# Optimization experiments

Measured on AMD Instinct MI355X. Metric: run time of the kernel, lower is better.

The kernel has to match this reference:

```python
import jax, jax.numpy as jnp
import numpy as np

B, S, D, H, E, K = 4, 1024, 1024, 16, 8, 2
DH = D // H
FF = 4 * D  # expert hidden dim
EPS = 1e-5


def _layernorm(x, g, b):
    mu = jnp.mean(x, axis=-1, keepdims=True)
    var = jnp.mean(jnp.square(x - mu), axis=-1, keepdims=True)
    return (x - mu) / jnp.sqrt(var + EPS) * g + b


def setup_inputs() -> dict:
    key = jax.random.key(0)
    ks = jax.random.split(key, 16)
    s = 0.02
    return {
        "x": jax.random.normal(ks[0], (B, S, D), jnp.float32),
        "mask": jnp.ones((B, S), jnp.int32),
        "ln1_g": jnp.ones((D,), jnp.float32),
        "ln1_b": jnp.zeros((D,), jnp.float32),
        "ln2_g": jnp.ones((D,), jnp.float32),
        "ln2_b": jnp.zeros((D,), jnp.float32),
        "wq": jax.random.normal(ks[1], (D, D), jnp.float32) * s,
        "bq": jnp.zeros((D,), jnp.float32),
        "wk": jax.random.normal(ks[2], (D, D), jnp.float32) * s,
        "bk": jnp.zeros((D,), jnp.float32),
        "wv": jax.random.normal(ks[3], (D, D), jnp.float32) * s,
        "bv": jnp.zeros((D,), jnp.float32),
        "wo": jax.random.normal(ks[4], (D, D), jnp.float32) * s,
        "bo": jnp.zeros((D,), jnp.float32),
        "w_router": jax.random.normal(ks[5], (D, E), jnp.float32) * s,
        "b_router": jnp.zeros((E,), jnp.float32),
        "w1": jax.random.normal(ks[6], (E, D, FF), jnp.float32) * s,
        "b1": jnp.zeros((E, FF), jnp.float32),
        "w2": jax.random.normal(ks[7], (E, FF, D), jnp.float32) * s,
        "b2": jnp.zeros((E, D), jnp.float32),
    }


def _forward(x, mask, ln1_g, ln1_b, ln2_g, ln2_b, wq, bq, wk, bk, wv, bv,
             wo, bo, w_router, b_router, w1, b1, w2, b2):
    scale = DH ** -0.5
    # --- attention sub-block (pre-LN) ---
    xn = _layernorm(x, ln1_g, ln1_b)
    q = (xn @ wq + bq).reshape(B, S, H, DH).transpose(0, 2, 1, 3)  # [B,H,S,DH]
    k = (xn @ wk + bk).reshape(B, S, H, DH).transpose(0, 2, 1, 3)
    v = (xn @ wv + bv).reshape(B, S, H, DH).transpose(0, 2, 1, 3)
    scores = jnp.einsum('bhqd,bhkd->bhqk', q, k) * scale
    scores = jnp.where(mask[:, None, None, :] == 0, -jnp.inf, scores)
    attn = jax.nn.softmax(scores, axis=-1)
    ao = jnp.einsum('bhqk,bhkd->bhqd', attn, v)
    ao = ao.transpose(0, 2, 1, 3).reshape(B, S, D) @ wo + bo
    x = x + ao  # dropout is identity in eval
    # --- MoE sub-block ---
    xn2 = _layernorm(x, ln2_g, ln2_b)
    logits = xn2 @ w_router + b_router          # [B,S,E]
    top_v, top_i = jax.lax.top_k(logits, K)     # [B,S,K]
    probs = jax.nn.softmax(top_v, axis=-1)      # softmax over top-k logits
    # dense combine weight per expert: sum_k prob_k * onehot(idx_k)
    combine = jnp.sum(jax.nn.one_hot(top_i, E, dtype=xn2.dtype) * probs[..., None], axis=-2)  # [B,S,E]
    h = jax.nn.gelu(jnp.einsum('bsd,edh->ebsh', xn2, w1) + b1[:, None, None, :], approximate=False)
    eo = jnp.einsum('ebsh,ehd->ebsd', h, w2) + b2[:, None, None, :]   # [E,B,S,D]
    moe_out = jnp.einsum('bse,ebsd->bsd', combine, eo)
    return x + moe_out


def reference(x, mask, ln1_g, ln1_b, ln2_g, ln2_b, wq, bq, wk, bk, wv, bv,
              wo, bo, w_router, b_router, w1, b1, w2, b2):
    return _forward(x, mask, ln1_g, ln1_b, ln2_g, ln2_b, wq, bq, wk, bk, wv,
                    bv, wo, bo, w_router, b_router, w1, b1, w2, b2)
```

## Files before the change

### kernel.cpp

```cpp
#include <hip/hip_runtime.h>
#include <hip/hip_bf16.h>
#include <cmath>

typedef __hip_bfloat16 bf16;
typedef float f32x4 __attribute__((ext_vector_type(4)));
typedef int   i32x4 __attribute__((ext_vector_type(4)));

#define DEV static __device__ __forceinline__

constexpr int BB   = 4;
constexpr int SS   = 1024;
constexpr int DM   = 1024;
constexpr int HH   = 16;
constexpr int DHD  = 64;
constexpr int NEXP = 8;
constexpr int FFD  = 4096;
constexpr int NTOK = BB*SS;
constexpr int CAP  = NTOK*2 + NEXP*128;

DEV float bf2f(unsigned short u){ union{unsigned int i; float f;} z; z.i=((unsigned int)u)<<16; return z.f; }
DEV unsigned short f2bf(float f){ bf16 h = __float2bfloat16(f); return __builtin_bit_cast(unsigned short, h); }

DEV void stage16(const void* g, void* lds_base_uniform) {
  __builtin_amdgcn_global_load_lds(
      (const __attribute__((address_space(1))) void*)g,
      (__attribute__((address_space(3))) void*)lds_base_uniform,
      16, 0, 0);
}

template<int BM,int BN,int EPI,bool EXPERT,bool GATHER,bool OUT_SLOT,int NPASS=1,int ZMODE=0>
__global__ __launch_bounds__((BM/64)*(BN/64)*64)
void et_gemm(const bf16* __restrict__ A, const bf16* __restrict__ Bt, void* __restrict__ Cout,
             const float* __restrict__ bias, const float* __restrict__ res,
             int Kdim, int lda, int ldb, int ldc,
             long abs_, long bbs_, long cbs_, float scale,
             const int* __restrict__ pad_off, const int* __restrict__ slots,
             long psA, long psB, float* __restrict__ Cf, int bias_zs)
{
  constexpr int WN = BN/64, WM = BM/64, NW = WM*WN;
  constexpr int CA = (BM/16)/NW, CB = (BN/16)/NW;
  const int tid = threadIdx.x, wid = tid>>6, lane = tid&63;

  const int gx = gridDim.x, gy = gridDim.y;
  const long nwg = (long)gx*gy*gridDim.z;
  long lin = blockIdx.x + (long)gx*(blockIdx.y + (long)gy*blockIdx.z);
  {
    const long q = nwg >> 3, r = nwg & 7;
    const long xcd = lin & 7, idx = lin >> 3;
    lin = (xcd < r ? xcd*(q+1) : r*(q+1) + (xcd-r)*q) + idx;
  }
  const int bxi = (int)(lin % gx);
  const long rem = lin / gx;
  const int byi = (int)(rem % gy);
  const int bzi = (int)(rem / gy);

  const int row0 = bxi*BM, col0 = byi*BN;
  const int z = bzi;
  int off0 = 0;
  if constexpr (EXPERT) {
    off0 = pad_off[z];
    const int rows = pad_off[z+1] - off0;
    if (row0 >= rows) return;
  }
  long coff;
  if constexpr (ZMODE==1) {
    const long hb = (long)(z>>4)*SS*DM + (long)(z&15)*64;
    A += hb; Bt += hb; coff = (long)z*SS*SS;
  } else if constexpr (ZMODE==2) {
    A  += (long)z*SS*SS;
    Bt += (long)z*DHD*SS;
    coff = (long)(z>>4)*SS*DM + (long)(z&15)*64;
  } else {
    if constexpr (!EXPERT) A += (size_t)z * abs_;
    Bt += (size_t)z * bbs_;
    coff = (long)z*cbs_;
  }
  const long bofs = (long)z * bias_zs;

  __shared__ __align__(16) bf16 As[2][BM*32];
  __shared__ __align__(16) bf16 Bs[2][BN*32];

  const int sr = lane>>2;
  const int sk = (lane&3)*8;

  long arow[CA];
  #pragma unroll
  for (int i=0;i<CA;i++){
    const int r = (wid + i*NW)*16 + sr;
    if constexpr (GATHER)      arow[i] = slots[off0 + row0 + r];
    else if constexpr (EXPERT) arow[i] = off0 + row0 + r;
    else                       arow[i] = row0 + r;
  }
  int brow[CB];
  #pragma unroll
  for (int i=0;i<CB;i++) brow[i] = col0 + (wid + i*NW)*16 + sr;

  const int wm = wid / WN, wn = wid % WN;
  const int fr = lane & 15, fg = lane >> 4;

  f32x4 acc[4][4];
  #pragma unroll
  for (int m=0;m<4;m++)
    #pragma unroll
    for (int n=0;n<4;n++) acc[m][n] = (f32x4)(0.f);

  static constexpr int AI[3]={0,0,1};
  static constexpr int BI[3]={0,1,0};

  auto STAGE = [&](int buf, int p, int kt) {
    const bf16* Ap = A  + (long)AI[p]*psA;
    const bf16* Bp = Bt + (long)BI[p]*psB;
    #pragma unroll
    for (int i=0;i<CA;i++)
      stage16(Ap + arow[i]*(long)lda + kt + sk, (void*)&As[buf][(wid + i*NW)*512]);
    #pragma unroll
    for (int i=0;i<CB;i++)
      stage16(Bp + (long)brow[i]*ldb + kt + sk, (void*)&Bs[buf][(wid + i*NW)*512]);
  };

  const int nsteps = NPASS * (Kdim >> 5);
  int cur = 0;
  int np = 0, nk = 0;
  STAGE(0, 0, 0);
  nk = 32;
  __syncthreads();

  for (int s = 0; s < nsteps; s++) {
    if (s + 1 < nsteps) {
      if (nk == Kdim) { nk = 0; np++; }
      STAGE(cur^1, np, nk);
      nk += 32;
    }
    i32x4 av[4], bv[4];
    #pragma unroll
    for (int m=0;m<4;m++) av[m] = *(const i32x4*)&As[cur][(wm*64 + m*16 + fr)*32 + fg*8];
    #pragma unroll
    for (int n=0;n<4;n++) bv[n] = *(const i32x4*)&Bs[cur][(wn*64 + n*16 + fr)*32 + fg*8];
    asm volatile("s_nop 1" ::);
    #pragma unroll
    for (int m=0;m<4;m++)
      #pragma unroll
      for (int n=0;n<4;n++)
        asm("v_mfma_f32_16x16x32_bf16 %0, %1, %2, %0"
            : "+v"(acc[m][n]) : "v"(av[m]), "v"(bv[n]));
    __syncthreads();
    cur ^= 1;
  }

  #pragma unroll
  for (int m=0;m<4;m++)
    #pragma unroll
    for (int n=0;n<4;n++)
      asm volatile("s_nop 7\n\ts_nop 7" : "+v"(acc[m][n]) ::);

  const long rbase = (EXPERT && OUT_SLOT) ? (long)(off0 + row0) : (long)row0;
  #pragma unroll
  for (int m=0;m<4;m++) {
    #pragma unroll
    for (int n=0;n<4;n++) {
      #pragma unroll
      for (int j=0;j<4;j++) {
        const long r = rbase + wm*64 + m*16 + fg*4 + j;
        const long c = col0 + wn*64 + n*16 + fr;
        const size_t ci = (size_t)coff + (size_t)r*ldc + c;
        float v = acc[m][n][j];
        if constexpr (EPI==0) {
          ((bf16*)Cout)[ci] = __float2bfloat16(v + bias[bofs + c]);
        } else if constexpr (EPI==1) {
          ((bf16*)Cout)[ci] = __float2bfloat16(v*scale);
        } else if constexpr (EPI==2) {
          ((float*)Cout)[ci] = v + bias[bofs + c] + res[(size_t)r*ldc + c];
        } else if constexpr (EPI==3) {
          const float t = v + bias[bofs + c];
          ((bf16*)Cout)[ci] = __float2bfloat16(0.5f*t*(1.0f+erff(t*0.70710678118654752f)));
        } else {
          const float t = v + bias[bofs + c];
          ((bf16*)Cout)[ci] = __float2bfloat16(t);
          Cf[ci] = t;
        }
      }
    }
  }
}

template<typename T>
__global__ __launch_bounds__(256)
void et_transpose(const T* __restrict__ in, bf16* __restrict__ outp,
                  int ldin, int ldout, long in_bs, long out_bs)
{
  __shared__ float tile[64][65];
  const int z = blockIdx.z;
  in   += (size_t)z * in_bs;
  outp += (size_t)z * out_bs;
  const int r0 = blockIdx.x*64, c0 = blockIdx.y*64;
  const int tid = threadIdx.x;
  #pragma unroll
  for (int i=0;i<4;i++) {
    const int idx = tid*4 + i*1024;
    const int r = idx>>6, c = idx&63;
    if constexpr (sizeof(T)==4) {
      const float4 v = *(const float4*)&in[(size_t)(r0+r)*ldin + c0 + c];
      tile[r][c]=v.x; tile[r][c+1]=v.y; tile[r][c+2]=v.z; tile[r][c+3]=v.w;
    } else {
      const ushort4 v = *(const ushort4*)&in[(size_t)(r0+r)*ldin + c0 + c];
      tile[r][c]=bf2f(v.x); tile[r][c+1]=bf2f(v.y); tile[r][c+2]=bf2f(v.z); tile[r][c+3]=bf2f(v.w);
    }
  }
  __syncthreads();
  #pragma unroll
  for (int i=0;i<4;i++) {
    const int idx = tid*4 + i*1024;
    const int c = idx>>6, r = idx&63;
    ushort4 o;
    o.x=f2bf(tile[r][c]); o.y=f2bf(tile[r+1][c]); o.z=f2bf(tile[r+2][c]); o.w=f2bf(tile[r+3][c]);
    *(ushort4*)&outp[(size_t)(c0+c)*ldout + r0 + r] = o;
  }
}

template<typename TI, typename TO>
__global__ __launch_bounds__(256)
void k_trans_head(const TI* __restrict__ in, TO* __restrict__ outp)
{
  __shared__ float tile[64][65];
  const int z = blockIdx.z;
  in   += (size_t)(z>>4)*SS*DM + (size_t)(z&15)*64;
  outp += (size_t)z*DHD*SS;
  const int r0 = blockIdx.x*64;
  const int tid = threadIdx.x;
  #pragma unroll
  for (int i=0;i<4;i++) {
    const int idx = tid*4 + i*1024;
    const int r = idx>>6, c = idx&63;
    if constexpr (sizeof(TI)==4) {
      const float4 v = *(const float4*)&in[(size_t)(r0+r)*DM + c];
      tile[r][c]=v.x; tile[r][c+1]=v.y; tile[r][c+2]=v.z; tile[r][c+3]=v.w;
    } else {
      const ushort4 v = *(const ushort4*)&in[(size_t)(r0+r)*DM + c];
      tile[r][c]=bf2f(v.x); tile[r][c+1]=bf2f(v.y); tile[r][c+2]=bf2f(v.z); tile[r][c+3]=bf2f(v.w);
    }
  }
  __syncthreads();
  #pragma unroll
  for (int i=0;i<4;i++) {
    const int idx = tid*4 + i*1024;
    const int c = idx>>6, r = idx&63;
    if constexpr (sizeof(TO)==4) {
      float4 o;
      o.x=tile[r][c]; o.y=tile[r+1][c]; o.z=tile[r+2][c]; o.w=tile[r+3][c];
      *(float4*)&outp[(size_t)c*SS + r0 + r] = o;
    } else {
      ushort4 o;
      o.x=f2bf(tile[r][c]); o.y=f2bf(tile[r+1][c]); o.z=f2bf(tile[r+2][c]); o.w=f2bf(tile[r+3][c]);
      *(ushort4*)&outp[(size_t)c*SS + r0 + r] = o;
    }
  }
}

__global__ __launch_bounds__(256)
void et_transpose2(const float* __restrict__ in, bf16* __restrict__ outp,
                   int ldin, int ldout, long pstride)
{
  __shared__ float tile[64][65];
  const int r0 = blockIdx.x*64, c0 = blockIdx.y*64;
  const int tid = threadIdx.x;
  #pragma unroll
  for (int i=0;i<4;i++) {
    const int idx = tid*4 + i*1024;
    const int r = idx>>6, c = idx&63;
    const float4 v = *(const float4*)&in[(size_t)(r0+r)*ldin + c0 + c];
    tile[r][c]=v.x; tile[r][c+1]=v.y; tile[r][c+2]=v.z; tile[r][c+3]=v.w;
  }
  __syncthreads();
  #pragma unroll
  for (int i=0;i<4;i++) {
    const int idx = tid*4 + i*1024;
    const int c = idx>>6, r = idx&63;
    ushort4 o0, o1;
    unsigned short* p0 = (unsigned short*)&o0;
    unsigned short* p1 = (unsigned short*)&o1;
    #pragma unroll
    for (int j=0;j<4;j++) {
      float v = tile[r+j][c];
      const unsigned short h0 = f2bf(v);
      p0[j] = h0;
      v -= bf2f(h0);
      p1[j] = f2bf(v);
    }
    const size_t oi = (size_t)(c0+c)*ldout + r0 + r;
    *(ushort4*)&outp[oi] = o0;
    *(ushort4*)&outp[oi + pstride] = o1;
  }
}

__global__ __launch_bounds__(256)
void et_ln2(const float* __restrict__ xin, const float* __restrict__ g,
            const float* __restrict__ bsh, bf16* __restrict__ outp, long pstride)
{
  const int row = blockIdx.x, tid = threadIdx.x;
  const float4 v = ((const float4*)(xin + (size_t)row*DM))[tid];
  float s = v.x+v.y+v.z+v.w;
  #pragma unroll
  for (int o=32;o;o>>=1) s += __shfl_xor(s,o);
  __shared__ float s4[4], q4[4];
  if ((tid&63)==0) s4[tid>>6]=s;
  __syncthreads();
  const float mu = (s4[0]+s4[1]+s4[2]+s4[3]) * (1.f/DM);
  const float d0=v.x-mu,d1=v.y-mu,d2=v.z-mu,d3=v.w-mu;
  float q = d0*d0+d1*d1+d2*d2+d3*d3;
  #pragma unroll
  for (int o=32;o;o>>=1) q += __shfl_xor(q,o);
  if ((tid&63)==0) q4[tid>>6]=q;
  __syncthreads();
  const float var = (q4[0]+q4[1]+q4[2]+q4[3]) * (1.f/DM);
  const float rstd = rsqrtf(var + 1e-5f);
  const float4 gg = ((const float4*)g)[tid];
  const float4 bb = ((const float4*)bsh)[tid];
  float of[4];
  of[0] = d0*rstd*gg.x + bb.x;
  of[1] = d1*rstd*gg.y + bb.y;
  of[2] = d2*rstd*gg.z + bb.z;
  of[3] = d3*rstd*gg.w + bb.w;
  ushort4 p0, p1;
  unsigned short* pp0 = (unsigned short*)&p0;
  unsigned short* pp1 = (unsigned short*)&p1;
  #pragma unroll
  for (int k=0;k<4;k++) {
    float vv = of[k];
    const unsigned short h0 = f2bf(vv); pp0[k] = h0;
    vv -= bf2f(h0);
    pp1[k] = f2bf(vv);
  }
  const size_t oi = (size_t)row*DM;
  ((ushort4*)(outp + oi))[tid] = p0;
  ((ushort4*)(outp + pstride + oi))[tid] = p1;
}

__global__ __launch_bounds__(256)
void et_ln(const float* __restrict__ xin, const float* __restrict__ g,
           const float* __restrict__ bsh, bf16* __restrict__ outp)
{
  const int row = blockIdx.x, tid = threadIdx.x;
  const float4 v = ((const float4*)(xin + (size_t)row*DM))[tid];
  float s = v.x+v.y+v.z+v.w;
  #pragma unroll
  for (int o=32;o;o>>=1) s += __shfl_xor(s,o);
  __shared__ float s4[4], q4[4];
  if ((tid&63)==0) s4[tid>>6]=s;
  __syncthreads();
  const float mu = (s4[0]+s4[1]+s4[2]+s4[3]) * (1.f/DM);
  const float d0=v.x-mu,d1=v.y-mu,d2=v.z-mu,d3=v.w-mu;
  float q = d0*d0+d1*d1+d2*d2+d3*d3;
  #pragma unroll
  for (int o=32;o;o>>=1) q += __shfl_xor(q,o);
  if ((tid&63)==0) q4[tid>>6]=q;
  __syncthreads();
  const float var = (q4[0]+q4[1]+q4[2]+q4[3]) * (1.f/DM);
  const float rstd = rsqrtf(var + 1e-5f);
  const float4 gg = ((const float4*)g)[tid];
  const float4 bb = ((const float4*)bsh)[tid];
  ushort4 o4;
  o4.x = f2bf(d0*rstd*gg.x + bb.x);
  o4.y = f2bf(d1*rstd*gg.y + bb.y);
  o4.z = f2bf(d2*rstd*gg.z + bb.z);
  o4.w = f2bf(d3*rstd*gg.w + bb.w);
  ((ushort4*)(outp + (size_t)row*DM))[tid] = o4;
}

__global__ __launch_bounds__(256)
void et_softmax(bf16* __restrict__ scp, const int* __restrict__ mask)
{
  const int row = blockIdx.x, tid = threadIdx.x;
  const int b = row >> 14;
  bf16* rp = scp + (size_t)row*SS;
  const int* mrow = mask + (size_t)b*SS;
  const ushort4 u = ((const ushort4*)rp)[tid];
  const int4 mv = ((const int4*)mrow)[tid];
  float f0 = bf2f(u.x), f1 = bf2f(u.y), f2 = bf2f(u.z), f3 = bf2f(u.w);
  if (mv.x==0) f0 = -1e30f;
  if (mv.y==0) f1 = -1e30f;
  if (mv.z==0) f2 = -1e30f;
  if (mv.w==0) f3 = -1e30f;
  float m = fmaxf(fmaxf(f0,f1),fmaxf(f2,f3));
  #pragma unroll
  for (int o=32;o;o>>=1) m = fmaxf(m, __shfl_xor(m,o));
  __shared__ float sm[4], ssum[4];
  if ((tid&63)==0) sm[tid>>6] = m;
  __syncthreads();
  m = fmaxf(fmaxf(sm[0],sm[1]),fmaxf(sm[2],sm[3]));
  const float e0 = __expf(f0-m), e1 = __expf(f1-m), e2 = __expf(f2-m), e3 = __expf(f3-m);
  float s = e0+e1+e2+e3;
  #pragma unroll
  for (int o=32;o;o>>=1) s += __shfl_xor(s,o);
  if ((tid&63)==0) ssum[tid>>6] = s;
  __syncthreads();
  s = ssum[0]+ssum[1]+ssum[2]+ssum[3];
  const float ri = 1.0f/s;
  ushort4 o4;
  o4.x = f2bf(e0*ri); o4.y = f2bf(e1*ri); o4.z = f2bf(e2*ri); o4.w = f2bf(e3*ri);
  ((ushort4*)rp)[tid] = o4;
}

__global__ __launch_bounds__(256)
void et_router2(const float* __restrict__ x1, const float* __restrict__ g,
                const float* __restrict__ bsh, const float* __restrict__ wr,
                const float* __restrict__ br, int* __restrict__ t2e,
                float* __restrict__ t2p, int* __restrict__ flaglist,
                int* __restrict__ cntb)
{
  const int wid = threadIdx.x>>6, lane = threadIdx.x&63;
  const int t = blockIdx.x*4 + wid;
  const float* xr = x1 + (size_t)t*DM;
  float4 xv[4];
  float s = 0.f;
  #pragma unroll
  for (int p=0;p<4;p++){
    xv[p] = *(const float4*)&xr[p*256 + lane*4];
    s += xv[p].x+xv[p].y+xv[p].z+xv[p].w;
  }
  #pragma unroll
  for (int o=32;o;o>>=1) s += __shfl_xor(s,o);
  const float mu = s * (1.f/DM);
  float q = 0.f;
  #pragma unroll
  for (int p=0;p<4;p++){
    const float a=xv[p].x-mu,b=xv[p].y-mu,c=xv[p].z-mu,d=xv[p].w-mu;
    q += a*a+b*b+c*c+d*d;
  }
  #pragma unroll
  for (int o=32;o;o>>=1) q += __shfl_xor(q,o);
  const float rstd = rsqrtf(q*(1.f/DM) + 1e-5f);
  float acc[NEXP];
  #pragma unroll
  for (int e=0;e<NEXP;e++) acc[e]=0.f;
  #pragma unroll
  for (int p=0;p<4;p++){
    const int d0 = p*256 + lane*4;
    const float4 gg = *(const float4*)&g[d0];
    const float4 bb = *(const float4*)&bsh[d0];
    float xn[4];
    xn[0]=(xv[p].x-mu)*rstd*gg.x+bb.x;
    xn[1]=(xv[p].y-mu)*rstd*gg.y+bb.y;
    xn[2]=(xv[p].z-mu)*rstd*gg.z+bb.z;
    xn[3]=(xv[p].w-mu)*rstd*gg.w+bb.w;
    #pragma unroll
    for (int j=0;j<4;j++){
      const float4 w0  = ((const float4*)&wr[(size_t)(d0+j)*NEXP])[0];
      const float4 w1v = ((const float4*)&wr[(size_t)(d0+j)*NEXP])[1];
      acc[0]+=xn[j]*w0.x;  acc[1]+=xn[j]*w0.y;  acc[2]+=xn[j]*w0.z;  acc[3]+=xn[j]*w0.w;
      acc[4]+=xn[j]*w1v.x; acc[5]+=xn[j]*w1v.y; acc[6]+=xn[j]*w1v.z; acc[7]+=xn[j]*w1v.w;
    }
  }
  #pragma unroll
  for (int e=0;e<NEXP;e++)
    #pragma unroll
    for (int o=32;o;o>>=1) acc[e] += __shfl_xor(acc[e],o);
  if (lane==0) {
    float v0=-1e30f, v1=-1e30f, v2=-1e30f; int e0=0, e1=0;
    #pragma unroll
    for (int e=0;e<NEXP;e++) {
      const float v = acc[e] + br[e];
      if (v>v0){v2=v1;v1=v0;e1=e0;v0=v;e0=e;}
      else if (v>v1){v2=v1;v1=v;e1=e;}
      else if (v>v2){v2=v;}
    }
    const float dd = __expf(v1-v0);
    const float p0 = 1.f/(1.f+dd);
    t2e[t*2]=e0; t2e[t*2+1]=e1;
    t2p[t*2]=p0; t2p[t*2+1]=dd*p0;
    if (v1 - v2 < 0.02f) {
      const int b = t >> 10;
      const int ib = atomicAdd(&cntb[b], 1);
      flaglist[b*1024 + ib] = t;
    }
  }
}

__global__ __launch_bounds__(256)
void k_rec4(const float* __restrict__ qf, const float* __restrict__ kfT,
            const float* __restrict__ vf, const int* __restrict__ flaglist,
            const int* __restrict__ cntb, const int* __restrict__ mask,
            float* __restrict__ aoF)
{
  const int h = blockIdx.y, b = blockIdx.z;
  const int tid = threadIdx.x, lane = tid&63, wv_ = tid>>6;
  const int nb = cntb[b];
  __shared__ float qs[4][64];
  __shared__ float scb[4][SS];
  __shared__ float part[4][4][64];
  __shared__ float tsum[4];
  const int* mrow = mask + (size_t)b*SS;
  const float* kbase = kfT + ((size_t)(b*HH + h)*DHD)*SS + tid;
  const float* vbase = vf + (size_t)b*SS*DM + h*64 + lane;

  for (int t0 = blockIdx.x*4; t0 < nb; t0 += gridDim.x*4) {
    const int nt = min(4, nb - t0);
    for (int idx = tid; idx < 4*64; idx += 256) {
      const int j = idx >> 6, d = idx & 63;
      float qv = 0.f;
      if (j < nt) {
        const int t = flaglist[b*1024 + t0 + j];
        qv = qf[(size_t)t*DM + h*64 + d];
      }
      qs[j][d] = qv;
    }
    __syncthreads();
    float a00=0,a01=0,a02=0,a03=0, a10=0,a11=0,a12=0,a13=0;
    float a20=0,a21=0,a22=0,a23=0, a30=0,a31=0,a32=0,a33=0;
    #pragma unroll 4
    for (int u=0; u<64; u++) {
      const float* kr = kbase + (size_t)u*SS;
      const float k0 = kr[0], k1 = kr[256], k2 = kr[512], k3 = kr[768];
      const float q0 = qs[0][u], q1 = qs[1][u], q2 = qs[2][u], q3 = qs[3][u];
      a00 += q0*k0; a01 += q0*k1; a02 += q0*k2; a03 += q0*k3;
      a10 += q1*k0; a11 += q1*k1; a12 += q1*k2; a13 += q1*k3;
      a20 += q2*k0; a21 += q2*k1; a22 += q2*k2; a23 += q2*k3;
      a30 += q3*k0; a31 += q3*k1; a32 += q3*k2; a33 += q3*k3;
    }
    const bool m0 = mrow[tid]!=0, m1 = mrow[tid+256]!=0, m2 = mrow[tid+512]!=0, m3 = mrow[tid+768]!=0;
    scb[0][tid]=m0?a00*0.125f:-1e30f; scb[0][tid+256]=m1?a01*0.125f:-1e30f;
    scb[0][tid+512]=m2?a02*0.125f:-1e30f; scb[0][tid+768]=m3?a03*0.125f:-1e30f;
    scb[1][tid]=m0?a10*0.125f:-1e30f; scb[1][tid+256]=m1?a11*0.125f:-1e30f;
    scb[1][tid+512]=m2?a12*0.125f:-1e30f; scb[1][tid+768]=m3?a13*0.125f:-1e30f;
    scb[2][tid]=m0?a20*0.125f:-1e30f; scb[2][tid+256]=m1?a21*0.125f:-1e30f;
    scb[2][tid+512]=m2?a22*0.125f:-1e30f; scb[2][tid+768]=m3?a23*0.125f:-1e30f;
    scb[3][tid]=m0?a30*0.125f:-1e30f; scb[3][tid+256]=m1?a31*0.125f:-1e30f;
    scb[3][tid+512]=m2?a32*0.125f:-1e30f; scb[3][tid+768]=m3?a33*0.125f:-1e30f;
    __syncthreads();
    {
      const int j = wv_;
      float v[16];
      float lm = -1e30f;
      #pragma unroll
      for (int kk=0;kk<16;kk++) { v[kk] = scb[j][lane + kk*64]; lm = fmaxf(lm, v[kk]); }
      #pragma unroll
      for (int o=32;o;o>>=1) lm = fmaxf(lm, __shfl_xor(lm,o));
      float ls = 0.f;
      #pragma unroll
      for (int kk=0;kk<16;kk++) {
        const float e = expf(v[kk]-lm);
        scb[j][lane + kk*64] = e; ls += e;
      }
      #pragma unroll
      for (int o=32;o;o>>=1) ls += __shfl_xor(ls,o);
      if (lane==0) tsum[j] = ls;
    }
    __syncthreads();
    float p0=0.f, p1=0.f, p2=0.f, p3=0.f;
    for (int s = wv_*4; s < SS; s += 16) {
      const float v0 = vbase[(size_t) s   *DM];
      const float v1 = vbase[(size_t)(s+1)*DM];
      const float v2 = vbase[(size_t)(s+2)*DM];
      const float v3 = vbase[(size_t)(s+3)*DM];
      p0 += scb[0][s]*v0 + scb[0][s+1]*v1 + scb[0][s+2]*v2 + scb[0][s+3]*v3;
      p1 += scb[1][s]*v0 + scb[1][s+1]*v1 + scb[1][s+2]*v2 + scb[1][s+3]*v3;
      p2 += scb[2][s]*v0 + scb[2][s+1]*v1 + scb[2][s+2]*v2 + scb[2][s+3]*v3;
      p3 += scb[3][s]*v0 + scb[3][s+1]*v1 + scb[3][s+2]*v2 + scb[3][s+3]*v3;
    }
    part[wv_][0][lane] = p0;
    part[wv_][1][lane] = p1;
    part[wv_][2][lane] = p2;
    part[wv_][3][lane] = p3;
    __syncthreads();
    for (int idx = tid; idx < nt*64; idx += 256) {
      const int j = idx >> 6, d = idx & 63;
      aoF[(size_t)(b*1024 + t0 + j)*DM + h*64 + d] =
        (part[0][j][d]+part[1][j][d]+part[2][j][d]+part[3][j][d]) / tsum[j];
    }
    __syncthreads();
  }
}

__global__ __launch_bounds__(256)
void k_flag_proj2(const float* __restrict__ aoF, const float* __restrict__ wo,
                  const float* __restrict__ bo, const float* __restrict__ x,
                  const int* __restrict__ flaglist, const int* __restrict__ cntb,
                  float* __restrict__ yF)
{
  const int tile = blockIdx.x;
  const int b = tile >> 7;
  const int i0 = (tile & 127) * 8;
  const int nb = cntb[b];
  if (i0 >= nb) return;
  const int nt = min(8, nb - i0);
  const int c0 = blockIdx.y * 128;
  const int tid = threadIdx.x;
  const int c = c0 + (tid & 127);
  const int dh = tid >> 7;
  __shared__ float ar[8][DM];
  __shared__ float ph[2][8][128];
  for (int k = tid; k < 8*256; k += 256) {
    const int j = k >> 8, q4i = k & 255;
    float4 v = make_float4(0.f,0.f,0.f,0.f);
    if (j < nt) v = ((const float4*)(aoF + (size_t)(b*1024 + i0 + j)*DM))[q4i];
    ((float4*)ar[j])[q4i] = v;
  }
  __syncthreads();
  float acc0=0.f, acc1=0.f, acc2=0.f, acc3=0.f;
  float acc4=0.f, acc5=0.f, acc6=0.f, acc7=0.f;
  const int dbase = dh*512;
  #pragma unroll 4
  for (int d=0; d<512; d++) {
    const float w = wo[(size_t)(dbase+d)*DM + c];
    acc0 += ar[0][dbase+d]*w; acc1 += ar[1][dbase+d]*w;
    acc2 += ar[2][dbase+d]*w; acc3 += ar[3][dbase+d]*w;
    acc4 += ar[4][dbase+d]*w; acc5 += ar[5][dbase+d]*w;
    acc6 += ar[6][dbase+d]*w; acc7 += ar[7][dbase+d]*w;
  }
  const int lc = tid & 127;
  ph[dh][0][lc]=acc0; ph[dh][1][lc]=acc1; ph[dh][2][lc]=acc2; ph[dh][3][lc]=acc3;
  ph[dh][4][lc]=acc4; ph[dh][5][lc]=acc5; ph[dh][6][lc]=acc6; ph[dh][7][lc]=acc7;
  __syncthreads();
  for (int k = tid; k < nt*128; k += 256) {
    const int j = k >> 7, ccl = k & 127;
    const int cc = c0 + ccl;
    const int slot = b*1024 + i0 + j;
    const int t = flaglist[slot];
    yF[(size_t)slot*DM + cc] = ph[0][j][ccl] + ph[1][j][ccl] + bo[cc] + x[(size_t)t*DM + cc];
  }
}

__global__ __launch_bounds__(256)
void k_flag_router(const float* __restrict__ yF, const float* __restrict__ g,
                   const float* __restrict__ bsh, const float* __restrict__ wr,
                   const float* __restrict__ br, const int* __restrict__ flaglist,
                   const int* __restrict__ cntb, int* __restrict__ t2e,
                   float* __restrict__ t2p)
{
  const int tid = threadIdx.x, lane = tid&63, wv_ = tid>>6;
  __shared__ float s4[4], q4[4], pt[4][8];
  for (int idx = blockIdx.x; idx < NTOK; idx += gridDim.x) {
    const int b = idx >> 10, ib = idx & 1023;
    if (ib >= cntb[b]) continue;
    const int t = flaglist[idx];
    const float4 v = ((const float4*)(yF + (size_t)idx*DM))[tid];
    float s = v.x+v.y+v.z+v.w;
    #pragma unroll
    for (int o=32;o;o>>=1) s += __shfl_xor(s,o);
    if (lane==0) s4[wv_]=s;
    __syncthreads();
    const float mu = (s4[0]+s4[1]+s4[2]+s4[3])*(1.f/DM);
    const float d0=v.x-mu, d1=v.y-mu, d2=v.z-mu, d3=v.w-mu;
    float q = d0*d0+d1*d1+d2*d2+d3*d3;
    #pragma unroll
    for (int o=32;o;o>>=1) q += __shfl_xor(q,o);
    if (lane==0) q4[wv_]=q;
    __syncthreads();
    const float var = (q4[0]+q4[1]+q4[2]+q4[3])*(1.f/DM);
    const float rstd = 1.0f/sqrtf(var + 1e-5f);
    const int dbase = tid*4;
    const float4 gg = ((const float4*)g)[tid];
    const float4 bb = ((const float4*)bsh)[tid];
    const float x0 = d0*rstd*gg.x+bb.x, x1_ = d1*rstd*gg.y+bb.y;
    const float x2 = d2*rstd*gg.z+bb.z, x3_ = d3*rstd*gg.w+bb.w;
    float pl[8];
    #pragma unroll
    for (int e=0;e<8;e++)
      pl[e] = x0*wr[(size_t)(dbase+0)*8+e] + x1_*wr[(size_t)(dbase+1)*8+e]
            + x2*wr[(size_t)(dbase+2)*8+e] + x3_*wr[(size_t)(dbase+3)*8+e];
    #pragma unroll
    for (int e=0;e<8;e++)
      #pragma unroll
      for (int o=32;o;o>>=1) pl[e] += __shfl_xor(pl[e],o);
    if (lane==0) {
      #pragma unroll
      for (int e=0;e<8;e++) pt[wv_][e]=pl[e];
    }
    __syncthreads();
    if (tid==0) {
      float v0=-1e30f, v1=-1e30f; int e0=0, e1=0;
      for (int e=0;e<8;e++) {
        const float L = pt[0][e]+pt[1][e]+pt[2][e]+pt[3][e] + br[e];
        if (L>v0){v1=v0;e1=e0;v0=L;e0=e;}
        else if (L>v1){v1=L;e1=e;}
      }
      const float dd=expf(v1-v0), p0=1.f/(1.f+dd);
      t2e[t*2]=e0; t2e[t*2+1]=e1;
      t2p[t*2]=p0; t2p[t*2+1]=dd*p0;
    }
    __syncthreads();
  }
}

__global__ void et_zero(int* cnt){ if (threadIdx.x < 16) cnt[threadIdx.x]=0; }

__global__ void et_bcat(const float* __restrict__ bq, const float* __restrict__ bk,
                        const float* __restrict__ bv, float* __restrict__ bcat)
{
  const int i = blockIdx.x*256 + threadIdx.x;
  if (i < DM) { bcat[i]=bq[i]; bcat[DM+i]=bk[i]; bcat[2*DM+i]=bv[i]; }
}

__global__ void et_count(const int* __restrict__ t2e, int* __restrict__ cnt)
{
  const int t = blockIdx.x*256 + threadIdx.x;
  if (t < NTOK) {
    atomicAdd(&cnt[t2e[t*2]], 1);
    atomicAdd(&cnt[t2e[t*2+1]], 1);
  }
}

__global__ void et_scan(const int* __restrict__ cnt, int* __restrict__ poff,
                        int* __restrict__ fil, int* __restrict__ slots)
{
  const int tid = threadIdx.x;
  if (tid==0) {
    int o=0;
    for (int e=0;e<NEXP;e++){ poff[e]=o; o += ((cnt[e]+127)>>7)<<7; }
    poff[NEXP]=o;
  }
  if (tid<NEXP) fil[tid]=0;
  for (int i=tid;i<CAP;i+=256) slots[i]=0;
}

__global__ void et_fill(const int* __restrict__ t2e, const int* __restrict__ poff,
                        int* __restrict__ fil, int* __restrict__ slots, int* __restrict__ sof)
{
  const int t = blockIdx.x*256 + threadIdx.x;
  if (t >= NTOK) return;
  #pragma unroll
  for (int kk=0;kk<2;kk++) {
    const int e = t2e[t*2+kk];
    const int pos = atomicAdd(&fil[e], 1);
    const int sl = poff[e] + pos;
    slots[sl] = t;
    sof[t*2+kk] = sl;
  }
}

__global__ __launch_bounds__(256)
void et_combine(const float* __restrict__ x1, const bf16* __restrict__ eo,
                const float* __restrict__ t2p, const int* __restrict__ sof,
                float* __restrict__ outp)
{
  const int t = blockIdx.x, tid = threadIdx.x;
  const int s0 = sof[t*2], s1 = sof[t*2+1];
  const float p0 = t2p[t*2], p1 = t2p[t*2+1];
  const float4 xv = ((const float4*)(x1 + (size_t)t*DM))[tid];
  const ushort4 a = ((const ushort4*)(eo + (size_t)s0*DM))[tid];
  const ushort4 c = ((const ushort4*)(eo + (size_t)s1*DM))[tid];
  float4 o;
  o.x = xv.x + p0*bf2f(a.x) + p1*bf2f(c.x);
  o.y = xv.y + p0*bf2f(a.y) + p1*bf2f(c.y);
  o.z = xv.z + p0*bf2f(a.z) + p1*bf2f(c.z);
  o.w = xv.w + p0*bf2f(a.w) + p1*bf2f(c.w);
  ((float4*)(outp + (size_t)t*DM))[tid] = o;
}

extern "C" void kernel_launch(void* const* d_in, const int* in_sizes, int n_in,
                              void* d_out, int out_size, void* d_ws, size_t ws_size,
                              hipStream_t stream)
{
  (void)in_sizes; (void)n_in; (void)out_size; (void)ws_size;
  const float* x    = (const float*)d_in[0];
  const int*   mask = (const int*)  d_in[1];
  const float* ln1g = (const float*)d_in[2];
  const float* ln1b = (const float*)d_in[3];
  const float* ln2g = (const float*)d_in[4];
  const float* ln2b = (const float*)d_in[5];
  const float* wq   = (const float*)d_in[6];
  const float* bq   = (const float*)d_in[7];
  const float* wk   = (const float*)d_in[8];
  const float* bk   = (const float*)d_in[9];
  const float* wv   = (const float*)d_in[10];
  const float* bv   = (const float*)d_in[11];
  const float* wo   = (const float*)d_in[12];
  const float* bo   = (const float*)d_in[13];
  const float* wr   = (const float*)d_in[14];
  const float* br   = (const float*)d_in[15];
  const float* w1   = (const float*)d_in[16];
  const float* b1   = (const float*)d_in[17];
  const float* w2   = (const float*)d_in[18];
  const float* b2   = (const float*)d_in[19];
  float* outp = (float*)d_out;

  char* wsb = (char*)d_ws;
  size_t off = 0;
  auto alloc = [&](size_t bytes)->void* {
    void* p = wsb + off;
    off += (bytes + 255) & ~(size_t)255;
    return p;
  };
  const long WPS  = (long)DM*DM;
  const long XPS  = (long)NTOK*DM;
  const long EWS  = (long)DM*FFD;
  bf16*  wqT2  = (bf16*) alloc((size_t)2*WPS*2);
  bf16*  wkT2  = (bf16*) alloc((size_t)2*WPS*2);
  bf16*  wvT2  = (bf16*) alloc((size_t)2*WPS*2);
  bf16*  woT   = (bf16*) alloc((size_t)WPS*2);
  bf16*  w1Ta  = (bf16*) alloc((size_t)NEXP*EWS*2);
  bf16*  w2Ta  = (bf16*) alloc((size_t)NEXP*EWS*2);
  bf16*  xn2p  = (bf16*) alloc((size_t)2*XPS*2);
  bf16*  qb    = (bf16*) alloc((size_t)XPS*2);
  bf16*  kb    = (bf16*) alloc((size_t)XPS*2);
  bf16*  vb    = (bf16*) alloc((size_t)XPS*2);
  bf16*  vt    = (bf16*) alloc((size_t)XPS*2);
  float* qf    = (float*)alloc((size_t)XPS*4);
  float* kf    = (float*)alloc((size_t)XPS*4);
  float* vf    = (float*)alloc((size_t)XPS*4);
  float* kfT   = (float*)alloc((size_t)XPS*4);
  bf16*  aob   = (bf16*) alloc((size_t)XPS*2);
  float* x1    = (float*)alloc((size_t)XPS*4);
  bf16*  xn2   = (bf16*) alloc((size_t)XPS*2);
  bf16*  hbuf  = (bf16*) alloc((size_t)CAP*FFD*2);
  bf16*  eo    = (bf16*) alloc((size_t)CAP*DM*2);
  float* bcat  = (float*)alloc((size_t)3*DM*4);
  int*   t2e   = (int*)  alloc((size_t)NTOK*2*4);
  float* t2p   = (float*)alloc((size_t)NTOK*2*4);
  int*   slots = (int*)  alloc((size_t)CAP*4);
  int*   sof   = (int*)  alloc((size_t)NTOK*2*4);
  int*   flagl = (int*)  alloc((size_t)NTOK*4);
  int*   cnt   = (int*)  alloc(64);
  int*   fil   = (int*)  alloc(64);
  int*   poff  = (int*)  alloc(64);
  int*   cntb  = cnt + 8;
  bf16*  sc    = (bf16*) w1Ta;
  float* aoF   = (float*)qb;
  float* yF    = (float*)vb;

  const dim3 T256(256);

  et_zero<<<1,64,0,stream>>>(cnt);
  et_bcat<<<4,T256,0,stream>>>(bq, bk, bv, bcat);
  et_transpose2<<<dim3(DM/64,DM/64),T256,0,stream>>>(wq, wqT2, DM, DM, WPS);
  et_transpose2<<<dim3(DM/64,DM/64),T256,0,stream>>>(wk, wkT2, DM, DM, WPS);
  et_transpose2<<<dim3(DM/64,DM/64),T256,0,stream>>>(wv, wvT2, DM, DM, WPS);
  et_transpose<float><<<dim3(DM/64,DM/64,1),T256,0,stream>>>(wo, woT, DM, DM, 0, 0);

  et_ln2<<<NTOK,T256,0,stream>>>(x, ln1g, ln1b, xn2p, XPS);

  et_gemm<128,64,4,false,false,false,3,0><<<dim3(NTOK/128, DM/64, 3),dim3(128),0,stream>>>(
      xn2p, wqT2, qb, bcat, nullptr, DM, DM, DM, DM,
      0, 2*WPS, XPS, 1.f, nullptr, nullptr, XPS, WPS, qf, DM);

  k_trans_head<bf16,bf16><<<dim3(SS/64,1,BB*HH),T256,0,stream>>>(vb, vt);
  k_trans_head<float,float><<<dim3(SS/64,1,BB*HH),T256,0,stream>>>(kf, kfT);

  et_gemm<128,128,1,false,false,false,1,1><<<dim3(SS/128, SS/128, BB*HH),T256,0,stream>>>(
      qb, kb, sc, nullptr, nullptr, DHD, DM, DM, SS,
      0,0,0, 0.125f, nullptr,nullptr, 0,0,nullptr, 0);
  et_softmax<<<BB*HH*SS,T256,0,stream>>>(sc, mask);
  et_gemm<128,64,1,false,false,false,1,2><<<dim3(SS/128, 1, BB*HH),dim3(128),0,stream>>>(
      sc, vt, aob, nullptr, nullptr, SS, SS, SS, DM,
      0,0,0, 1.0f, nullptr,nullptr, 0,0,nullptr, 0);

  et_gemm<128,128,2,false,false,false,1,0><<<dim3(NTOK/128, DM/128, 1),T256,0,stream>>>(
      aob, woT, x1, bo, x, DM, DM, DM, DM, 0,0,0, 1.f, nullptr,nullptr, 0,0,nullptr, 0);
  et_ln<<<NTOK,T256,0,stream>>>(x1, ln2g, ln2b, xn2);

  et_router2<<<NTOK/4,T256,0,stream>>>(x1, ln2g, ln2b, wr, br, t2e, t2p, flagl, cntb);
  k_rec4<<<dim3(32,HH,BB),T256,0,stream>>>(qf, kfT, vf, flagl, cntb, mask, aoF);
  k_flag_proj2<<<dim3(NTOK/8, DM/128),T256,0,stream>>>(aoF, wo, bo, x, flagl, cntb, yF);
  k_flag_router<<<1024,T256,0,stream>>>(yF, ln2g, ln2b, wr, br, flagl, cntb, t2e, t2p);

  et_count<<<NTOK/256,T256,0,stream>>>(t2e, cnt);
  et_scan<<<1,T256,0,stream>>>(cnt, poff, fil, slots);
  et_fill<<<NTOK/256,T256,0,stream>>>(t2e, poff, fil, slots, sof);

  et_transpose<float><<<dim3(DM/64, FFD/64, NEXP),T256,0,stream>>>(w1, w1Ta, FFD, DM, EWS, EWS);
  et_transpose<float><<<dim3(FFD/64, DM/64, NEXP),T256,0,stream>>>(w2, w2Ta, DM, FFD, EWS, EWS);

  et_gemm<128,128,3,true,true,true,1,0><<<dim3(NTOK/128, FFD/128, NEXP),T256,0,stream>>>(
      xn2, w1Ta, hbuf, b1, nullptr, DM, DM, DM, FFD,
      0, EWS, 0, 1.f, poff, slots, 0,0,nullptr, FFD);
  et_gemm<128,128,0,true,false,true,1,0><<<dim3(NTOK/128, DM/128, NEXP),T256,0,stream>>>(
      hbuf, w2Ta, eo, b2, nullptr, FFD, FFD, FFD, DM,
      0, EWS, 0, 1.f, poff, nullptr, 0,0,nullptr, DM);

  et_combine<<<NTOK,T256,0,stream>>>(x1, eo, t2p, sof, outp);
}
```

Measured before the change: 954.3 us.

## Triple-buffer GEMM LDS staging and fuse second layernorm into router

The shared GEMM kernel moves from double to triple-buffered LDS staging. It uses explicit vmcnt waits and raw s_barrier, so two K-tiles are in flight while the current one is computed, which should hide more global load latency. Separately, the standalone second layernorm kernel is removed and the router kernel now writes the bf16 normalized activations itself, saving a launch and a read of x1. The extra LDS buffer raises shared memory per block and may reduce occupancy.

```diff
diff --git a/kernel.cpp b/kernel.cpp
--- a/kernel.cpp
+++ b/kernel.cpp
@@ -28,6 +28,15 @@
       16, 0, 0);
 }
 
+template<int N> DEV void wait_vmcnt() {
+  if constexpr (N==0)      asm volatile("s_waitcnt vmcnt(0)" ::: "memory");
+  else if constexpr (N==4) asm volatile("s_waitcnt vmcnt(4)" ::: "memory");
+  else if constexpr (N==6) asm volatile("s_waitcnt vmcnt(6)" ::: "memory");
+  else if constexpr (N==8) asm volatile("s_waitcnt vmcnt(8)" ::: "memory");
+  else                     asm volatile("s_waitcnt vmcnt(12)" ::: "memory");
+}
+DEV void block_bar(){ asm volatile("s_barrier" ::: "memory"); }
+
 template<int BM,int BN,int EPI,bool EXPERT,bool GATHER,bool OUT_SLOT,int NPASS=1,int ZMODE=0>
 __global__ __launch_bounds__((BM/64)*(BN/64)*64)
 void et_gemm(const bf16* __restrict__ A, const bf16* __restrict__ Bt, void* __restrict__ Cout,
@@ -39,6 +48,7 @@
 {
   constexpr int WN = BN/64, WM = BM/64, NW = WM*WN;
   constexpr int CA = (BM/16)/NW, CB = (BN/16)/NW;
+  constexpr int LPT = CA + CB;
   const int tid = threadIdx.x, wid = tid>>6, lane = tid&63;
 
   const int gx = gridDim.x, gy = gridDim.y;
@@ -77,8 +87,8 @@
   }
   const long bofs = (long)z * bias_zs;
 
-  __shared__ __align__(16) bf16 As[2][BM*32];
-  __shared__ __align__(16) bf16 Bs[2][BN*32];
+  __shared__ __align__(16) bf16 As[3][BM*32];
+  __shared__ __align__(16) bf16 Bs[3][BN*32];
 
   const int sr = lane>>2;
   const int sk = (lane&3)*8;
@@ -107,29 +117,31 @@
   static constexpr int AI[3]={0,0,1};
   static constexpr int BI[3]={0,1,0};
 
-  auto STAGE = [&](int buf, int p, int kt) {
-    const bf16* Ap = A  + (long)AI[p]*psA;
-    const bf16* Bp = Bt + (long)BI[p]*psB;
+  int np = 0, nk = 0;
+  auto STAGE = [&](int buf) {
+    const bf16* Ap = A  + (long)AI[np]*psA;
+    const bf16* Bp = Bt + (long)BI[np]*psB;
     #pragma unroll
     for (int i=0;i<CA;i++)
-      stage16(Ap + arow[i]*(long)lda + kt + sk, (void*)&As[buf][(wid + i*NW)*512]);
+      stage16(Ap + arow[i]*(long)lda + nk + sk, (void*)&As[buf][(wid + i*NW)*512]);
     #pragma unroll
     for (int i=0;i<CB;i++)
-      stage16(Bp + (long)brow[i]*ldb + kt + sk, (void*)&Bs[buf][(wid + i*NW)*512]);
+      stage16(Bp + (long)brow[i]*ldb + nk + sk, (void*)&Bs[buf][(wid + i*NW)*512]);
+    nk += 32;
+    if (nk == Kdim) { nk = 0; np++; }
   };
 
   const int nsteps = NPASS * (Kdim >> 5);
-  int cur = 0;
-  int np = 0, nk = 0;
-  STAGE(0, 0, 0);
-  nk = 32;
-  __syncthreads();
-
+  STAGE(0);
+  if (nsteps > 1) { STAGE(1); wait_vmcnt<LPT>(); }
+  else            { wait_vmcnt<0>(); }
+  block_bar();
+
+  int cur = 0, sb = 2;
   for (int s = 0; s < nsteps; s++) {
-    if (s + 1 < nsteps) {
-      if (nk == Kdim) { nk = 0; np++; }
-      STAGE(cur^1, np, nk);
-      nk += 32;
+    if (s + 2 < nsteps) {
+      STAGE(sb);
+      sb = (sb==2) ? 0 : sb+1;
     }
     i32x4 av[4], bv[4];
     #pragma unroll
@@ -143,8 +155,10 @@
       for (int n=0;n<4;n++)
         asm("v_mfma_f32_16x16x32_bf16 %0, %1, %2, %0"
             : "+v"(acc[m][n]) : "v"(av[m]), "v"(bv[n]));
-    __syncthreads();
-    cur ^= 1;
+    if (s + 2 < nsteps)      wait_vmcnt<LPT>();
+    else if (s + 1 < nsteps) wait_vmcnt<0>();
+    if (s + 1 < nsteps) block_bar();
+    cur = (cur==2) ? 0 : cur+1;
   }
 
   #pragma unroll
@@ -336,37 +350,6 @@
 }
 
 __global__ __launch_bounds__(256)
-void et_ln(const float* __restrict__ xin, const float* __restrict__ g,
-           const float* __restrict__ bsh, bf16* __restrict__ outp)
-{
-  const int row = blockIdx.x, tid = threadIdx.x;
-  const float4 v = ((const float4*)(xin + (size_t)row*DM))[tid];
-  float s = v.x+v.y+v.z+v.w;
-  #pragma unroll
-  for (int o=32;o;o>>=1) s += __shfl_xor(s,o);
-  __shared__ float s4[4], q4[4];
-  if ((tid&63)==0) s4[tid>>6]=s;
-  __syncthreads();
-  const float mu = (s4[0]+s4[1]+s4[2]+s4[3]) * (1.f/DM);
-  const float d0=v.x-mu,d1=v.y-mu,d2=v.z-mu,d3=v.w-mu;
-  float q = d0*d0+d1*d1+d2*d2+d3*d3;
-  #pragma unroll
-  for (int o=32;o;o>>=1) q += __shfl_xor(q,o);
-  if ((tid&63)==0) q4[tid>>6]=q;
-  __syncthreads();
-  const float var = (q4[0]+q4[1]+q4[2]+q4[3]) * (1.f/DM);
-  const float rstd = rsqrtf(var + 1e-5f);
-  const float4 gg = ((const float4*)g)[tid];
-  const float4 bb = ((const float4*)bsh)[tid];
-  ushort4 o4;
-  o4.x = f2bf(d0*rstd*gg.x + bb.x);
-  o4.y = f2bf(d1*rstd*gg.y + bb.y);
-  o4.z = f2bf(d2*rstd*gg.z + bb.z);
-  o4.w = f2bf(d3*rstd*gg.w + bb.w);
-  ((ushort4*)(outp + (size_t)row*DM))[tid] = o4;
-}
-
-__global__ __launch_bounds__(256)
 void et_softmax(bf16* __restrict__ scp, const int* __restrict__ mask)
 {
   const int row = blockIdx.x, tid = threadIdx.x;
@@ -403,9 +386,9 @@
 __global__ __launch_bounds__(256)
 void et_router2(const float* __restrict__ x1, const float* __restrict__ g,
                 const float* __restrict__ bsh, const float* __restrict__ wr,
-                const float* __restrict__ br, int* __restrict__ t2e,
-                float* __restrict__ t2p, int* __restrict__ flaglist,
-                int* __restrict__ cntb)
+                const float* __restrict__ br, bf16* __restrict__ xn2,
+                int* __restrict__ t2e, float* __restrict__ t2p,
+                int* __restrict__ flaglist, int* __restrict__ cntb)
 {
   const int wid = threadIdx.x>>6, lane = threadIdx.x&63;
   const int t = blockIdx.x*4 + wid;
@@ -442,6 +425,9 @@
     xn[1]=(xv[p].y-mu)*rstd*gg.y+bb.y;
     xn[2]=(xv[p].z-mu)*rstd*gg.z+bb.z;
     xn[3]=(xv[p].w-mu)*rstd*gg.w+bb.w;
+    ushort4 xo;
+    xo.x=f2bf(xn[0]); xo.y=f2bf(xn[1]); xo.z=f2bf(xn[2]); xo.w=f2bf(xn[3]);
+    *(ushort4*)&xn2[(size_t)t*DM + d0] = xo;
     #pragma unroll
     for (int j=0;j<4;j++){
       const float4 w0  = ((const float4*)&wr[(size_t)(d0+j)*NEXP])[0];
@@ -845,9 +831,8 @@
 
   et_gemm<128,128,2,false,false,false,1,0><<<dim3(NTOK/128, DM/128, 1),T256,0,stream>>>(
       aob, woT, x1, bo, x, DM, DM, DM, DM, 0,0,0, 1.f, nullptr,nullptr, 0,0,nullptr, 0);
-  et_ln<<<NTOK,T256,0,stream>>>(x1, ln2g, ln2b, xn2);
-
-  et_router2<<<NTOK/4,T256,0,stream>>>(x1, ln2g, ln2b, wr, br, t2e, t2p, flagl, cntb);
+
+  et_router2<<<NTOK/4,T256,0,stream>>>(x1, ln2g, ln2b, wr, br, xn2, t2e, t2p, flagl, cntb);
   k_rec4<<<dim3(32,HH,BB),T256,0,stream>>>(qf, kfT, vf, flagl, cntb, mask, aoF);
   k_flag_proj2<<<dim3(NTOK/8, DM/128),T256,0,stream>>>(aoF, wo, bo, x, flagl, cntb, yF);
   k_flag_router<<<1024,T256,0,stream>>>(yF, ln2g, ln2b, wr, br, flagl, cntb, t2e, t2p);
```

After: 1.025 ms. 7.4% more time.
